# Kernel tuning notes

Hardware: AMD Instinct MI355X
Metric: run time of the kernel (lower is better)

Reference implementation:

```python
import jax, jax.numpy as jnp
import numpy as np

DIM = 256
HEADS = 4
HEAD_DIM = DIM // HEADS
MLP_HIDDEN = DIM * 3
B, N = 8, 4096
EPS = 1e-5


def setup_inputs() -> dict:
    key = jax.random.key(0)
    ks = jax.random.split(key, 8)
    s = 0.02
    return {
        "x": jax.random.normal(ks[0], (B, N, DIM), dtype=jnp.float32),
        "w_qkv": jax.random.normal(ks[1], (DIM, 3 * DIM), dtype=jnp.float32) * s,
        "b_qkv": jnp.zeros((3 * DIM,), dtype=jnp.float32),
        "norm_g": jnp.ones((DIM,), dtype=jnp.float32),
        "norm_b": jnp.zeros((DIM,), dtype=jnp.float32),
        "w_fc1": jax.random.normal(ks[2], (DIM, MLP_HIDDEN), dtype=jnp.float32) * s,
        "b_fc1": jnp.zeros((MLP_HIDDEN,), dtype=jnp.float32),
        "w_fc2": jax.random.normal(ks[3], (MLP_HIDDEN, DIM), dtype=jnp.float32) * s,
        "b_fc2": jnp.zeros((DIM,), dtype=jnp.float32),
    }


def _layernorm(x, g, b):
    mu = jnp.mean(x, axis=-1, keepdims=True)
    var = jnp.mean(jnp.square(x - mu), axis=-1, keepdims=True)
    return (x - mu) * jax.lax.rsqrt(var + EPS) * g + b


def reference(x, w_qkv, b_qkv, norm_g, norm_b, w_fc1, b_fc1, w_fc2, b_fc2):
    Bx, Nx, C = x.shape
    scale = HEAD_DIM ** -0.5
    qkv = (x @ w_qkv + b_qkv).reshape(Bx, Nx, 3, HEADS, HEAD_DIM)
    qkv = jnp.transpose(qkv, (2, 0, 3, 1, 4))  # [3, B, H, N, hd]
    q, k, v = qkv[0], qkv[1], qkv[2]
    k = k * scale
    # channel attention: [B,H,hd,hd]
    attn = jnp.einsum('bhnd,bhne->bhde', k, v)
    attn = jax.nn.softmax(attn, axis=-1)
    # x_feature[b,h,n,d] = sum_e attn[b,h,d,e] * q[b,h,n,e]
    xf = jnp.einsum('bhde,bhne->bhnd', attn, q)
    xf = jnp.transpose(xf, (0, 2, 1, 3)).reshape(Bx, Nx, C)
    x = x + xf
    # FFN with residual (exact GELU as torch nn.GELU default)
    h = _layernorm(x, norm_g, norm_b)
    h = jax.nn.gelu(h @ w_fc1 + b_fc1, approximate=False) @ w_fc2 + b_fc2
    return x + h
```

## Files before the change

kernel.cpp:

```cpp
#include <hip/hip_runtime.h>
#include <math.h>

typedef __bf16 bf16_t;
typedef __bf16 bf16x4 __attribute__((ext_vector_type(4)));
typedef __bf16 bf16x8 __attribute__((ext_vector_type(8)));
typedef float f32x4 __attribute__((ext_vector_type(4)));

#define DIMC 256
#define HID 768
#define NB 8
#define NN 4096
#define ROWS (NB*NN)
#define NCHUNK 16

#define AS1 __attribute__((address_space(1)))
#define AS3 __attribute__((address_space(3)))

__device__ __forceinline__ void gll16(const bf16_t* src, void* lds) {
  __builtin_amdgcn_global_load_lds((const AS1 void*)src, (AS3 void*)lds, 16, 0, 0);
}

__global__ __launch_bounds__(256) void prep_x_kernel(const float* __restrict__ x,
                                                     bf16_t* __restrict__ xb) {
  int i = (blockIdx.x * 256 + threadIdx.x) * 8;
  f32x4 a = *(const f32x4*)(x + i);
  f32x4 b = *(const f32x4*)(x + i + 4);
  bf16x8 o;
  o[0] = (bf16_t)a[0]; o[1] = (bf16_t)a[1]; o[2] = (bf16_t)a[2]; o[3] = (bf16_t)a[3];
  o[4] = (bf16_t)b[0]; o[5] = (bf16_t)b[1]; o[6] = (bf16_t)b[2]; o[7] = (bf16_t)b[3];
  *(bf16x8*)(xb + i) = o;
}

__global__ __launch_bounds__(256)
void pack_w_kernel(const float* __restrict__ w, bf16_t* __restrict__ out,
                   int K, int Nw) {
  int idx = blockIdx.x * 256 + threadIdx.x;
  int lane = idx & 63;
  int kq = (idx >> 6) % (K >> 5);
  int nt = idx / ((K >> 5) << 6);
  int n = nt * 16 + (lane & 15);
  int k0 = kq * 32 + (lane >> 4) * 8;
  bf16x8 o;
#pragma unroll
  for (int j = 0; j < 8; ++j) o[j] = (bf16_t)w[(size_t)(k0 + j) * Nw + n];
  *(bf16x8*)(out + (size_t)idx * 8) = o;
}

__device__ __forceinline__ float gelu_exact(float v) {
  return 0.5f * v * (1.0f + erff(v * 0.70710678118654752f));
}

template <int EPI>
__global__ __launch_bounds__(256, 2)
void gemm_packed_kernel(const bf16_t* __restrict__ A, const bf16_t* __restrict__ Bp,
                        const float* __restrict__ bias, bf16_t* __restrict__ outp) {
  __shared__ __align__(16) unsigned char smem[32768];
  const int tid = threadIdx.x;
  const int m0 = blockIdx.y * 64;
  const int n0 = blockIdx.x * 192;
  const int lane = tid & 63, w = tid >> 6;
  const int lr = lane & 15, lk = lane >> 4;

#pragma unroll
  for (int i = 0; i < 8; ++i) {
    int idx = i * 256 + tid;
    int row = idx >> 5, pk = idx & 31;
    gll16(A + (size_t)(m0 + row) * 256 + ((pk ^ (row & 7)) * 8), smem + idx * 16);
  }
  asm volatile("s_waitcnt vmcnt(0)" ::: "memory");
  __builtin_amdgcn_s_barrier();

  f32x4 acc[4][3] = {};
  const bf16_t* bb = Bp + (size_t)((blockIdx.x * 12 + w * 3) * 8) * 512 + lane * 8;

#pragma unroll
  for (int kq = 0; kq < 8; ++kq) {
    bf16x8 bf[3];
#pragma unroll
    for (int nf = 0; nf < 3; ++nf)
      bf[nf] = *(const bf16x8*)(bb + (nf * 8 + kq) * 512);
    bf16x8 af[4];
#pragma unroll
    for (int mi = 0; mi < 4; ++mi) {
      int row = mi * 16 + lr;
      af[mi] = *(const bf16x8*)(smem + row * 512 + (((kq * 4 + lk) ^ (row & 7)) * 16));
    }
#pragma unroll
    for (int nf = 0; nf < 3; ++nf)
#pragma unroll
      for (int mi = 0; mi < 4; ++mi)
        acc[mi][nf] = __builtin_amdgcn_mfma_f32_16x16x32_bf16(bf[nf], af[mi],
                                                              acc[mi][nf], 0, 0, 0);
  }

  f32x4 bs[3];
#pragma unroll
  for (int nf = 0; nf < 3; ++nf)
    bs[nf] = *(const f32x4*)(bias + n0 + w * 48 + nf * 16 + lk * 4);

  __syncthreads();
#pragma unroll
  for (int mi = 0; mi < 4; ++mi) {
    int row_l = mi * 16 + lr;
#pragma unroll
    for (int nf = 0; nf < 3; ++nf) {
      int col = w * 48 + nf * 16 + lk * 4;
      f32x4 v = acc[mi][nf] + bs[nf];
      bf16x4 o;
#pragma unroll
      for (int r = 0; r < 4; ++r) {
        float val = v[r];
        if (EPI == 1) val = gelu_exact(val);
        o[r] = (bf16_t)val;
      }
      int chunk = col >> 3;
      int half = (col >> 2) & 1;
      *(bf16x4*)(smem + row_l * 384 + ((chunk ^ (row_l & 7)) << 4) + (half << 3)) = o;
    }
  }
  __syncthreads();
#pragma unroll
  for (int i = 0; i < 6; ++i) {
    int id = i * 256 + tid;
    int row_l = id / 24, c = id % 24;
    bf16x8 v = *(const bf16x8*)(smem + row_l * 384 + ((c ^ (row_l & 7)) << 4));
    *(bf16x8*)(outp + (size_t)(m0 + row_l) * 768 + n0 + c * 8) = v;
  }
}

__global__ __launch_bounds__(256, 2)
void fc2_packed_kernel(const bf16_t* __restrict__ mid, const bf16_t* __restrict__ Bp,
                       const float* __restrict__ bias, const bf16_t* __restrict__ resid,
                       float* __restrict__ outp) {
  __shared__ __align__(16) unsigned char smem[2 * 16384 + 32768];
  unsigned char* epi = smem + 32768;
  const int tid = threadIdx.x;
  const int m0 = blockIdx.x * 64;
  const int lane = tid & 63, w = tid >> 6;
  const int lr = lane & 15, lk = lane >> 4;

  auto stageA = [&](int c, int buf) {
#pragma unroll
    for (int i = 0; i < 4; ++i) {
      int idx = i * 256 + tid;
      int row = idx >> 4, pk = idx & 15;
      gll16(mid + (size_t)(m0 + row) * 768 + c * 128 + ((pk ^ (row & 7)) * 8),
            smem + buf * 16384 + idx * 16);
    }
  };

  stageA(0, 0);
  stageA(1, 1);
  asm volatile("s_waitcnt vmcnt(4)" ::: "memory");
  __builtin_amdgcn_s_barrier();

  f32x4 acc[4][4] = {};
#pragma unroll
  for (int c = 0; c < 6; ++c) {
    bf16x8 bf[4][4];
#pragma unroll
    for (int nf = 0; nf < 4; ++nf)
#pragma unroll
      for (int kql = 0; kql < 4; ++kql)
        bf[nf][kql] = *(const bf16x8*)(Bp + (size_t)((w * 4 + nf) * 24 + c * 4 + kql) * 512 + lane * 8);
    asm volatile("s_waitcnt vmcnt(0)" ::: "memory");
    __builtin_amdgcn_s_barrier();
#pragma unroll
    for (int kql = 0; kql < 4; ++kql) {
#pragma unroll
      for (int mi = 0; mi < 4; ++mi) {
        int row = mi * 16 + lr;
        bf16x8 a8 = *(const bf16x8*)(smem + (c & 1) * 16384 + row * 256 +
                                     (((kql * 4 + lk) ^ (row & 7)) * 16));
#pragma unroll
        for (int nf = 0; nf < 4; ++nf)
          acc[mi][nf] = __builtin_amdgcn_mfma_f32_16x16x32_bf16(bf[nf][kql], a8, acc[mi][nf], 0, 0, 0);
      }
    }
    __builtin_amdgcn_s_barrier();
    if (c + 2 < 6) stageA(c + 2, c & 1);
  }

  f32x4 bs[4];
#pragma unroll
  for (int nf = 0; nf < 4; ++nf)
    bs[nf] = *(const f32x4*)(bias + w * 64 + nf * 16 + lk * 4);

#pragma unroll
  for (int ph = 0; ph < 2; ++ph) {
    if (ph == 1) __syncthreads();
#pragma unroll
    for (int mj = 0; mj < 2; ++mj) {
      int mi = ph * 2 + mj;
      int row_l = mj * 16 + lr;
#pragma unroll
      for (int nf = 0; nf < 4; ++nf) {
        int cc = w * 64 + nf * 16 + lk * 4;
        f32x4 v = acc[mi][nf] + bs[nf];
        int chunk = cc >> 2;
        *(f32x4*)(epi + row_l * 1024 + ((chunk ^ (row_l & 7)) << 4)) = v;
      }
    }
    __syncthreads();
#pragma unroll
    for (int i = 0; i < 8; ++i) {
      int id = i * 256 + tid;
      int rl = id >> 6, c = id & 63;
      f32x4 v = *(const f32x4*)(epi + rl * 1024 + ((c ^ (rl & 7)) << 4));
      int grow = m0 + ph * 32 + rl;
      bf16x4 rz = *(const bf16x4*)(resid + (size_t)grow * 256 + c * 4);
#pragma unroll
      for (int r = 0; r < 4; ++r) v[r] += (float)rz[r];
      *(f32x4*)(outp + (size_t)grow * 256 + c * 4) = v;
    }
  }
}

__global__ __launch_bounds__(256)
void attn_kv_kernel(const bf16_t* __restrict__ qkv, float* __restrict__ part) {
  const int bh = blockIdx.x, chunk = blockIdx.y;
  const int b = bh >> 2, h = bh & 3;
  __shared__ __align__(16) float kl[32][68];
  __shared__ __align__(16) float vl[32][68];
  const int tid = threadIdx.x;
  const int dg = tid >> 4, eg = tid & 15;
  f32x4 acc[4] = {};
  const int n00 = chunk * (NN / NCHUNK);
  const int srow = tid >> 3, spk = tid & 7;
  for (int t = 0; t < (NN / NCHUNK) / 32; ++t) {
    int n0 = n00 + t * 32;
    {
      const bf16x8 k8 = *(const bf16x8*)(qkv + (size_t)(b * NN + n0 + srow) * HID + 256 + h * 64 + spk * 8);
      const bf16x8 v8 = *(const bf16x8*)(qkv + (size_t)(b * NN + n0 + srow) * HID + 512 + h * 64 + spk * 8);
#pragma unroll
      for (int j = 0; j < 8; ++j) kl[srow][spk * 8 + j] = (float)k8[j];
#pragma unroll
      for (int j = 0; j < 8; ++j) vl[srow][spk * 8 + j] = (float)v8[j];
    }
    __syncthreads();
#pragma unroll 8
    for (int n = 0; n < 32; ++n) {
      f32x4 k4 = *(const f32x4*)&kl[n][dg * 4];
      f32x4 v4 = *(const f32x4*)&vl[n][eg * 4];
#pragma unroll
      for (int i = 0; i < 4; ++i) acc[i] += k4[i] * v4;
    }
    __syncthreads();
  }
  float* dst = part + (size_t)(chunk * 32 + bh) * 4096;
#pragma unroll
  for (int i = 0; i < 4; ++i)
    *(f32x4*)&dst[(dg * 4 + i) * 64 + eg * 4] = acc[i];
}

__global__ __launch_bounds__(256)
void attn_softmax_kernel(const float* __restrict__ part, bf16_t* __restrict__ attnb) {
  const int bh = blockIdx.x;
  const int tid = threadIdx.x;
  const int dg = tid >> 4, eg = tid & 15;
  f32x4 s[4] = {};
  for (int c = 0; c < NCHUNK; ++c) {
    const float* src = part + (size_t)(c * 32 + bh) * 4096;
#pragma unroll
    for (int i = 0; i < 4; ++i) s[i] += *(const f32x4*)&src[(dg * 4 + i) * 64 + eg * 4];
  }
  bf16_t* dst = attnb + (size_t)bh * 4096;
#pragma unroll
  for (int i = 0; i < 4; ++i) {
    f32x4 l = s[i] * 0.125f;
    float m = fmaxf(fmaxf(l[0], l[1]), fmaxf(l[2], l[3]));
#pragma unroll
    for (int msk = 1; msk < 16; msk <<= 1) m = fmaxf(m, __shfl_xor(m, msk));
    f32x4 p;
    float sum = 0.f;
#pragma unroll
    for (int j = 0; j < 4; ++j) { p[j] = expf(l[j] - m); sum += p[j]; }
#pragma unroll
    for (int msk = 1; msk < 16; msk <<= 1) sum += __shfl_xor(sum, msk);
    float inv = 1.0f / sum;
    bf16x4 o;
#pragma unroll
    for (int j = 0; j < 4; ++j) o[j] = (bf16_t)(p[j] * inv);
    *(bf16x4*)&dst[(dg * 4 + i) * 64 + eg * 4] = o;
  }
}

__global__ __launch_bounds__(256, 2)
void xf_ln_mfma_kernel(const bf16_t* __restrict__ qkv, const bf16_t* __restrict__ attnb,
                       const bf16_t* __restrict__ xb, bf16_t* __restrict__ x2b,
                       bf16_t* __restrict__ hln, const float* __restrict__ gamma,
                       const float* __restrict__ beta) {
  __shared__ __align__(16) unsigned char qs[32768];
  __shared__ float red[4][4][16][2];
  const int tid = threadIdx.x;
  const int row0 = blockIdx.x * 64;
  const int b = row0 >> 12;
  const int lane = tid & 63, h = tid >> 6;
  const int lr = lane & 15, lk = lane >> 4;

#pragma unroll
  for (int i = 0; i < 8; ++i) {
    int idx = i * 256 + tid;
    int row = idx >> 5, pk = idx & 31;
    gll16(qkv + (size_t)(row0 + row) * HID + ((pk ^ (row & 7)) * 8), qs + idx * 16);
  }
  asm volatile("s_waitcnt vmcnt(0)" ::: "memory");
  __builtin_amdgcn_s_barrier();

  bf16x8 af[4][2];
#pragma unroll
  for (int mi = 0; mi < 4; ++mi)
#pragma unroll
    for (int kk = 0; kk < 2; ++kk) {
      int row = mi * 16 + lr;
      int pk = h * 8 + kk * 4 + lk;
      af[mi][kk] = *(const bf16x8*)(qs + row * 512 + ((pk ^ (row & 7)) * 16));
    }
  bf16x8 bfr[4][2];
#pragma unroll
  for (int nf = 0; nf < 4; ++nf)
#pragma unroll
    for (int kk = 0; kk < 2; ++kk)
      bfr[nf][kk] = *(const bf16x8*)(attnb + (size_t)(b * 4 + h) * 4096 +
                                     (nf * 16 + lr) * 64 + kk * 32 + lk * 8);
  f32x4 acc[4][4] = {};
#pragma unroll
  for (int kk = 0; kk < 2; ++kk)
#pragma unroll
    for (int mi = 0; mi < 4; ++mi)
#pragma unroll
      for (int nf = 0; nf < 4; ++nf)
        acc[mi][nf] = __builtin_amdgcn_mfma_f32_16x16x32_bf16(bfr[nf][kk], af[mi][kk], acc[mi][nf], 0, 0, 0);

  float ps[4], pq[4];
#pragma unroll
  for (int mi = 0; mi < 4; ++mi) {
    ps[mi] = 0.f; pq[mi] = 0.f;
    int row = row0 + mi * 16 + lr;
#pragma unroll
    for (int nf = 0; nf < 4; ++nf) {
      int col = h * 64 + nf * 16 + lk * 4;
      size_t off = (size_t)row * DIMC + col;
      bf16x4 xv = *(const bf16x4*)(xb + off);
      f32x4 x2;
#pragma unroll
      for (int r = 0; r < 4; ++r) {
        x2[r] = acc[mi][nf][r] + (float)xv[r];
        ps[mi] += x2[r]; pq[mi] += x2[r] * x2[r];
      }
      acc[mi][nf] = x2;
      bf16x4 o;
#pragma unroll
      for (int r = 0; r < 4; ++r) o[r] = (bf16_t)x2[r];
      *(bf16x4*)(x2b + off) = o;
    }
#pragma unroll
    for (int m = 16; m < 64; m <<= 1) {
      ps[mi] += __shfl_xor(ps[mi], m);
      pq[mi] += __shfl_xor(pq[mi], m);
    }
  }
  if (lk == 0) {
#pragma unroll
    for (int mi = 0; mi < 4; ++mi) { red[h][mi][lr][0] = ps[mi]; red[h][mi][lr][1] = pq[mi]; }
  }
  __builtin_amdgcn_s_barrier();
#pragma unroll
  for (int mi = 0; mi < 4; ++mi) {
    float t1 = red[0][mi][lr][0] + red[1][mi][lr][0] + red[2][mi][lr][0] + red[3][mi][lr][0];
    float t2 = red[0][mi][lr][1] + red[1][mi][lr][1] + red[2][mi][lr][1] + red[3][mi][lr][1];
    float mu = t1 * (1.0f / 256.0f);
    float var = t2 * (1.0f / 256.0f) - mu * mu;
    float rs = rsqrtf(var + 1e-5f);
    int row = row0 + mi * 16 + lr;
#pragma unroll
    for (int nf = 0; nf < 4; ++nf) {
      int col = h * 64 + nf * 16 + lk * 4;
      f32x4 g4 = *(const f32x4*)(gamma + col);
      f32x4 b4 = *(const f32x4*)(beta + col);
      bf16x4 o;
#pragma unroll
      for (int r = 0; r < 4; ++r)
        o[r] = (bf16_t)((acc[mi][nf][r] - mu) * rs * g4[r] + b4[r]);
      *(bf16x4*)(hln + (size_t)row * DIMC + col) = o;
    }
  }
}

extern "C" void kernel_launch(void* const* d_in, const int* in_sizes, int n_in,
                              void* d_out, int out_size, void* d_ws, size_t ws_size,
                              hipStream_t stream) {
  const float* x      = (const float*)d_in[0];
  const float* w_qkv  = (const float*)d_in[1];
  const float* b_qkv  = (const float*)d_in[2];
  const float* norm_g = (const float*)d_in[3];
  const float* norm_b = (const float*)d_in[4];
  const float* w_fc1  = (const float*)d_in[5];
  const float* b_fc1  = (const float*)d_in[6];
  const float* w_fc2  = (const float*)d_in[7];
  const float* b_fc2  = (const float*)d_in[8];

  char* ws = (char*)d_ws;
  size_t off = 0;
  bf16_t* qkv   = (bf16_t*)(ws + off); off += (size_t)ROWS * HID * 2;
  bf16_t* mid   = qkv;
  bf16_t* xb    = (bf16_t*)(ws + off); off += (size_t)ROWS * DIMC * 2;
  bf16_t* hln   = (bf16_t*)(ws + off); off += (size_t)ROWS * DIMC * 2;
  bf16_t* x2b   = (bf16_t*)(ws + off); off += (size_t)ROWS * DIMC * 2;
  float*  part  = (float*)(ws + off);  off += (size_t)NCHUNK * 32 * 4096 * 4;
  bf16_t* attnb = (bf16_t*)(ws + off); off += (size_t)32 * 4096 * 2;
  bf16_t* Bq    = (bf16_t*)(ws + off); off += (size_t)768 * 256 * 2;
  bf16_t* B1    = (bf16_t*)(ws + off); off += (size_t)768 * 256 * 2;
  bf16_t* B2    = (bf16_t*)(ws + off); off += (size_t)256 * 768 * 2;

  prep_x_kernel<<<(ROWS * DIMC) / (256 * 8), 256, 0, stream>>>(x, xb);
  pack_w_kernel<<<96, 256, 0, stream>>>(w_qkv, Bq, 256, 768);
  pack_w_kernel<<<96, 256, 0, stream>>>(w_fc1, B1, 256, 768);
  pack_w_kernel<<<96, 256, 0, stream>>>(w_fc2, B2, 768, 256);

  gemm_packed_kernel<0><<<dim3(4, ROWS / 64), 256, 0, stream>>>(xb, Bq, b_qkv, qkv);
  attn_kv_kernel<<<dim3(32, NCHUNK), 256, 0, stream>>>(qkv, part);
  attn_softmax_kernel<<<32, 256, 0, stream>>>(part, attnb);
  xf_ln_mfma_kernel<<<ROWS / 64, 256, 0, stream>>>(qkv, attnb, xb, x2b, hln, norm_g, norm_b);
  gemm_packed_kernel<1><<<dim3(4, ROWS / 64), 256, 0, stream>>>(hln, B1, b_fc1, mid);
  fc2_packed_kernel<<<ROWS / 64, 256, 0, stream>>>(mid, B2, b_fc2, x2b, (float*)d_out);
}
```

Before: 149.4 us.

## Fuse FC1+GELU and FC2 into one kernel keeping hidden activations in LDS

Replaces the separate FC1 GEMM (writing a 32768x768 bf16 intermediate to global memory) and the FC2 kernel with a single fused kernel. Each 64-row block loads its LayerNorm output into LDS, computes FC1 in 128-column chunks, applies bias and exact GELU, stores the chunk in LDS, and immediately accumulates it into FC2. This removes the global write and re-read of the hidden activation and one launch. In exchange it drops the async double-buffered staging, adds two barriers per chunk, and keeps more accumulators live, which may reduce overlap and occupancy.

```diff
diff --git a/kernel.cpp b/kernel.cpp
--- a/kernel.cpp
+++ b/kernel.cpp
@@ -129,62 +129,85 @@
 }
 
 __global__ __launch_bounds__(256, 2)
-void fc2_packed_kernel(const bf16_t* __restrict__ mid, const bf16_t* __restrict__ Bp,
-                       const float* __restrict__ bias, const bf16_t* __restrict__ resid,
-                       float* __restrict__ outp) {
-  __shared__ __align__(16) unsigned char smem[2 * 16384 + 32768];
-  unsigned char* epi = smem + 32768;
+void ffn_fused_kernel(const bf16_t* __restrict__ hln, const bf16_t* __restrict__ B1p,
+                      const float* __restrict__ b1, const bf16_t* __restrict__ B2p,
+                      const float* __restrict__ b2, const bf16_t* __restrict__ resid,
+                      float* __restrict__ outp) {
+  __shared__ __align__(16) unsigned char smem[32768 + 16384];
+  unsigned char* midl = smem + 32768;
   const int tid = threadIdx.x;
   const int m0 = blockIdx.x * 64;
   const int lane = tid & 63, w = tid >> 6;
   const int lr = lane & 15, lk = lane >> 4;
 
-  auto stageA = [&](int c, int buf) {
-#pragma unroll
-    for (int i = 0; i < 4; ++i) {
-      int idx = i * 256 + tid;
-      int row = idx >> 4, pk = idx & 15;
-      gll16(mid + (size_t)(m0 + row) * 768 + c * 128 + ((pk ^ (row & 7)) * 8),
-            smem + buf * 16384 + idx * 16);
-    }
-  };
-
-  stageA(0, 0);
-  stageA(1, 1);
-  asm volatile("s_waitcnt vmcnt(4)" ::: "memory");
+#pragma unroll
+  for (int i = 0; i < 8; ++i) {
+    int idx = i * 256 + tid;
+    int row = idx >> 5, pk = idx & 31;
+    gll16(hln + (size_t)(m0 + row) * 256 + ((pk ^ (row & 7)) * 8), smem + idx * 16);
+  }
+  asm volatile("s_waitcnt vmcnt(0)" ::: "memory");
   __builtin_amdgcn_s_barrier();
 
-  f32x4 acc[4][4] = {};
+  f32x4 acc2[4][4] = {};
 #pragma unroll
   for (int c = 0; c < 6; ++c) {
-    bf16x8 bf[4][4];
-#pragma unroll
-    for (int nf = 0; nf < 4; ++nf)
-#pragma unroll
-      for (int kql = 0; kql < 4; ++kql)
-        bf[nf][kql] = *(const bf16x8*)(Bp + (size_t)((w * 4 + nf) * 24 + c * 4 + kql) * 512 + lane * 8);
-    asm volatile("s_waitcnt vmcnt(0)" ::: "memory");
-    __builtin_amdgcn_s_barrier();
-#pragma unroll
-    for (int kql = 0; kql < 4; ++kql) {
+    f32x4 acc1[4][2] = {};
+#pragma unroll
+    for (int kq = 0; kq < 8; ++kq) {
+      bf16x8 bf1[2];
+#pragma unroll
+      for (int nf = 0; nf < 2; ++nf)
+        bf1[nf] = *(const bf16x8*)(B1p + (size_t)((c * 8 + w * 2 + nf) * 8 + kq) * 512 + lane * 8);
+      bf16x8 af[4];
 #pragma unroll
       for (int mi = 0; mi < 4; ++mi) {
         int row = mi * 16 + lr;
-        bf16x8 a8 = *(const bf16x8*)(smem + (c & 1) * 16384 + row * 256 +
-                                     (((kql * 4 + lk) ^ (row & 7)) * 16));
+        af[mi] = *(const bf16x8*)(smem + row * 512 + (((kq * 4 + lk) ^ (row & 7)) * 16));
+      }
+#pragma unroll
+      for (int nf = 0; nf < 2; ++nf)
+#pragma unroll
+        for (int mi = 0; mi < 4; ++mi)
+          acc1[mi][nf] = __builtin_amdgcn_mfma_f32_16x16x32_bf16(bf1[nf], af[mi],
+                                                                 acc1[mi][nf], 0, 0, 0);
+    }
+#pragma unroll
+    for (int mi = 0; mi < 4; ++mi) {
+      int row = mi * 16 + lr;
+#pragma unroll
+      for (int nf = 0; nf < 2; ++nf) {
+        int ck = w * 32 + nf * 16 + lk * 4;
+        f32x4 v = acc1[mi][nf] + *(const f32x4*)(b1 + c * 128 + ck);
+        bf16x4 o;
+#pragma unroll
+        for (int r = 0; r < 4; ++r) o[r] = (bf16_t)gelu_exact(v[r]);
+        *(bf16x4*)(midl + row * 256 + (((ck >> 3) ^ (row & 7)) << 4) + ((ck & 4) << 1)) = o;
+      }
+    }
+    __syncthreads();
+#pragma unroll
+    for (int kql = 0; kql < 4; ++kql) {
+      bf16x8 bf2[4];
+#pragma unroll
+      for (int nf = 0; nf < 4; ++nf)
+        bf2[nf] = *(const bf16x8*)(B2p + (size_t)((w * 4 + nf) * 24 + c * 4 + kql) * 512 + lane * 8);
+#pragma unroll
+      for (int mi = 0; mi < 4; ++mi) {
+        int row = mi * 16 + lr;
+        bf16x8 a8 = *(const bf16x8*)(midl + row * 256 + (((kql * 4 + lk) ^ (row & 7)) * 16));
 #pragma unroll
         for (int nf = 0; nf < 4; ++nf)
-          acc[mi][nf] = __builtin_amdgcn_mfma_f32_16x16x32_bf16(bf[nf][kql], a8, acc[mi][nf], 0, 0, 0);
-      }
-    }
-    __builtin_amdgcn_s_barrier();
-    if (c + 2 < 6) stageA(c + 2, c & 1);
-  }
-
-  f32x4 bs[4];
+          acc2[mi][nf] = __builtin_amdgcn_mfma_f32_16x16x32_bf16(bf2[nf], a8, acc2[mi][nf], 0, 0, 0);
+      }
+    }
+    __syncthreads();
+  }
+
+  f32x4 bs2[4];
 #pragma unroll
   for (int nf = 0; nf < 4; ++nf)
-    bs[nf] = *(const f32x4*)(bias + w * 64 + nf * 16 + lk * 4);
+    bs2[nf] = *(const f32x4*)(b2 + w * 64 + nf * 16 + lk * 4);
 
 #pragma unroll
   for (int ph = 0; ph < 2; ++ph) {
@@ -196,9 +219,9 @@
 #pragma unroll
       for (int nf = 0; nf < 4; ++nf) {
         int cc = w * 64 + nf * 16 + lk * 4;
-        f32x4 v = acc[mi][nf] + bs[nf];
+        f32x4 v = acc2[mi][nf] + bs2[nf];
         int chunk = cc >> 2;
-        *(f32x4*)(epi + row_l * 1024 + ((chunk ^ (row_l & 7)) << 4)) = v;
+        *(f32x4*)(smem + row_l * 1024 + ((chunk ^ (row_l & 7)) << 4)) = v;
       }
     }
     __syncthreads();
@@ -206,7 +229,7 @@
     for (int i = 0; i < 8; ++i) {
       int id = i * 256 + tid;
       int rl = id >> 6, c = id & 63;
-      f32x4 v = *(const f32x4*)(epi + rl * 1024 + ((c ^ (rl & 7)) << 4));
+      f32x4 v = *(const f32x4*)(smem + rl * 1024 + ((c ^ (rl & 7)) << 4));
       int grow = m0 + ph * 32 + rl;
       bf16x4 rz = *(const bf16x4*)(resid + (size_t)grow * 256 + c * 4);
 #pragma unroll
@@ -403,7 +426,6 @@
   char* ws = (char*)d_ws;
   size_t off = 0;
   bf16_t* qkv   = (bf16_t*)(ws + off); off += (size_t)ROWS * HID * 2;
-  bf16_t* mid   = qkv;
   bf16_t* xb    = (bf16_t*)(ws + off); off += (size_t)ROWS * DIMC * 2;
   bf16_t* hln   = (bf16_t*)(ws + off); off += (size_t)ROWS * DIMC * 2;
   bf16_t* x2b   = (bf16_t*)(ws + off); off += (size_t)ROWS * DIMC * 2;
@@ -422,6 +444,5 @@
   attn_kv_kernel<<<dim3(32, NCHUNK), 256, 0, stream>>>(qkv, part);
   attn_softmax_kernel<<<32, 256, 0, stream>>>(part, attnb);
   xf_ln_mfma_kernel<<<ROWS / 64, 256, 0, stream>>>(qkv, attnb, xb, x2b, hln, norm_g, norm_b);
-  gemm_packed_kernel<1><<<dim3(4, ROWS / 64), 256, 0, stream>>>(hln, B1, b_fc1, mid);
-  fc2_packed_kernel<<<ROWS / 64, 256, 0, stream>>>(mid, B2, b_fc2, x2b, (float*)d_out);
-}
+  ffn_fused_kernel<<<ROWS / 64, 256, 0, stream>>>(hln, B1, b_fc1, B2, b_fc2, x2b, (float*)d_out);
+}
```

New measurement: 150.1 us. Within noise of the previous version (+0.4%).

## Swizzle GEMM block order across XCDs and double-buffer fragment loads

Applied to the files above, without the earlier changes.

Remaps the linear block id so consecutive blocks are spread over the eight XCDs while blocks sharing an A row-tile and the four N panels land together, aiming for better L2 reuse. The k-loop now prefetches the next step's B fragments from global memory and A fragments from LDS into registers while issuing MFMAs on the current ones. It also raises wave priority around the MFMA burst. This adds register pressure under launch_bounds(256,2), and the remap assumes a 4x512 grid (the d&7 * 256 term).

```diff
diff --git a/kernel.cpp b/kernel.cpp
--- a/kernel.cpp
+++ b/kernel.cpp
@@ -56,8 +56,11 @@
                         const float* __restrict__ bias, bf16_t* __restrict__ outp) {
   __shared__ __align__(16) unsigned char smem[32768];
   const int tid = threadIdx.x;
-  const int m0 = blockIdx.y * 64;
-  const int n0 = blockIdx.x * 192;
+  const int d = blockIdx.x + blockIdx.y * 4;
+  const int w_ = (d & 7) * 256 + (d >> 3);
+  const int panel = w_ & 3, rowb = w_ >> 2;
+  const int m0 = rowb * 64;
+  const int n0 = panel * 192;
   const int lane = tid & 63, w = tid >> 6;
   const int lr = lane & 15, lk = lane >> 4;
 
@@ -71,26 +74,41 @@
   __builtin_amdgcn_s_barrier();
 
   f32x4 acc[4][3] = {};
-  const bf16_t* bb = Bp + (size_t)((blockIdx.x * 12 + w * 3) * 8) * 512 + lane * 8;
+  const bf16_t* bb = Bp + (size_t)((panel * 12 + w * 3) * 8) * 512 + lane * 8;
+
+  bf16x8 bf_c[3], af_c[4], bf_n[3], af_n[4];
+#pragma unroll
+  for (int nf = 0; nf < 3; ++nf) bf_c[nf] = *(const bf16x8*)(bb + (nf * 8) * 512);
+#pragma unroll
+  for (int mi = 0; mi < 4; ++mi) {
+    int row = mi * 16 + lr;
+    af_c[mi] = *(const bf16x8*)(smem + row * 512 + ((lk ^ (row & 7)) * 16));
+  }
 
 #pragma unroll
   for (int kq = 0; kq < 8; ++kq) {
-    bf16x8 bf[3];
+    if (kq < 7) {
+#pragma unroll
+      for (int nf = 0; nf < 3; ++nf)
+        bf_n[nf] = *(const bf16x8*)(bb + (nf * 8 + kq + 1) * 512);
+#pragma unroll
+      for (int mi = 0; mi < 4; ++mi) {
+        int row = mi * 16 + lr;
+        af_n[mi] = *(const bf16x8*)(smem + row * 512 + ((((kq + 1) * 4 + lk) ^ (row & 7)) * 16));
+      }
+    }
+    __builtin_amdgcn_s_setprio(1);
 #pragma unroll
     for (int nf = 0; nf < 3; ++nf)
-      bf[nf] = *(const bf16x8*)(bb + (nf * 8 + kq) * 512);
-    bf16x8 af[4];
-#pragma unroll
-    for (int mi = 0; mi < 4; ++mi) {
-      int row = mi * 16 + lr;
-      af[mi] = *(const bf16x8*)(smem + row * 512 + (((kq * 4 + lk) ^ (row & 7)) * 16));
-    }
-#pragma unroll
-    for (int nf = 0; nf < 3; ++nf)
 #pragma unroll
       for (int mi = 0; mi < 4; ++mi)
-        acc[mi][nf] = __builtin_amdgcn_mfma_f32_16x16x32_bf16(bf[nf], af[mi],
+        acc[mi][nf] = __builtin_amdgcn_mfma_f32_16x16x32_bf16(bf_c[nf], af_c[mi],
                                                               acc[mi][nf], 0, 0, 0);
+    __builtin_amdgcn_s_setprio(0);
+#pragma unroll
+    for (int nf = 0; nf < 3; ++nf) bf_c[nf] = bf_n[nf];
+#pragma unroll
+    for (int mi = 0; mi < 4; ++mi) af_c[mi] = af_n[mi];
   }
 
   f32x4 bs[3];
```

Measured after the change: 130.4 us. 1.15x faster.
